# Performance work log

Measured on AMD Instinct MI355X. Metric: run time of the kernel, lower is better.

Reference implementation:

```python
import jax, jax.numpy as jnp
import numpy as np

N, E, D_IN, LAT = 50000, 600000, 128, 64


def setup_inputs() -> dict:
    key = jax.random.key(0)
    ks = jax.random.split(key, 16)

    def w(k, i, o):
        return jax.random.normal(k, (i, o), jnp.float32) * (1.0 / np.sqrt(i))

    dims = [(D_IN, 64), (64, 128), (128, LAT)]
    inp = {
        "x": jax.random.normal(ks[0], (N, D_IN), jnp.float32),
        "edge_index": jax.random.randint(ks[1], (2, E), 0, N),
        "eps": jax.random.normal(ks[2], (N, LAT), jnp.float32),
    }
    for b_i, branch in enumerate(["mu", "ls"]):
        for li, (i, o) in enumerate(dims):
            inp[f"w_{branch}{li+1}"] = w(ks[3 + b_i * 3 + li], i, o)
            inp[f"b_{branch}{li+1}"] = jnp.zeros((o,), jnp.float32)
    return inp


def gcn(x, src, dst, dis, W, b):
    # GCNConv with add_self_loops=True and symmetric normalization:
    # out = D^-1/2 (A + I) D^-1/2 (x W) + b
    h = x @ W
    norm = dis[src] * dis[dst]                       # [E]
    agg = jax.ops.segment_sum(h[src] * norm[:, None], dst, num_segments=N)
    agg = agg + h * (dis * dis)[:, None]             # self-loop term d_i^-1 * h_i
    return agg + b


def encode_branch(x, src, dst, dis, ws, bs):
    h = x
    for W, b in zip(ws, bs):
        h = jax.nn.relu(gcn(h, src, dst, dis, W, b))  # ReLU after every GCNConv
    return h


def reference(x, edge_index, eps,
              w_mu1, b_mu1, w_mu2, b_mu2, w_mu3, b_mu3,
              w_ls1, b_ls1, w_ls2, b_ls2, w_ls3, b_ls3):
    src, dst = edge_index[0], edge_index[1]
    # degree with self loops (edge_weight = 1)
    deg = jax.ops.segment_sum(jnp.ones(E, x.dtype), dst, num_segments=N) + 1.0
    dis = jax.lax.rsqrt(deg)
    mu = encode_branch(x, src, dst, dis, [w_mu1, w_mu2, w_mu3], [b_mu1, b_mu2, b_mu3])
    logstd = encode_branch(x, src, dst, dis, [w_ls1, w_ls2, w_ls3], [b_ls1, b_ls2, b_ls3])
    logstd = jnp.minimum(logstd, 10.0)               # PyG VGAE MAX_LOGSTD clamp
    z = mu + eps * jnp.exp(logstd)                   # reparametrize (training=True)
    # VGAE inner-product decoder on observed edges, sigmoid=True
    adj = jax.nn.sigmoid(jnp.sum(z[src] * z[dst], axis=-1))
    return adj, mu, logstd
```

## Files before the change

### kernel.cpp

```cpp
#include <hip/hip_runtime.h>
#include <hip/hip_bf16.h>
#include <hip/hip_fp16.h>
#include <math.h>


__global__ void zero_int_k(int* __restrict__ p, int n) {
    int i = blockIdx.x * blockDim.x + threadIdx.x;
    if (i < n) p[i] = 0;
}

__global__ void count_dst_k(const int* __restrict__ ei, int* __restrict__ cnt, int E) {
    int e = blockIdx.x * blockDim.x + threadIdx.x;
    if (e < E) atomicAdd(&cnt[ei[E + e]], 1);
}

__global__ void compute_dis_k(const int* __restrict__ cnt, float* __restrict__ dis, int n) {
    int i = blockIdx.x * blockDim.x + threadIdx.x;
    if (i < n) dis[i] = rsqrtf((float)cnt[i] + 1.0f);
}

__global__ void scan1_k(const int* __restrict__ cnt, int* __restrict__ row_ptr,
                        int* __restrict__ bsum, int n) {
    __shared__ int wsum[16];
    int tid = threadIdx.x, lane = tid & 63, wv = tid >> 6;
    int i = blockIdx.x * 1024 + tid;
    int v = (i < n) ? cnt[i] : 0;
    int x = v;
#pragma unroll
    for (int off = 1; off < 64; off <<= 1) {
        int t = __shfl_up(x, off, 64);
        if (lane >= off) x += t;
    }
    if (lane == 63) wsum[wv] = x;
    __syncthreads();
    if (wv == 0 && lane < 16) {
        int y = wsum[lane];
#pragma unroll
        for (int off = 1; off < 16; off <<= 1) {
            int t = __shfl_up(y, off, 64);
            if (lane >= off) y += t;
        }
        wsum[lane] = y;
    }
    __syncthreads();
    int incl = x + ((wv == 0) ? 0 : wsum[wv - 1]);
    if (i < n) row_ptr[i + 1] = incl;
    if (tid == 1023) bsum[blockIdx.x] = incl;
}

__global__ void scan2_k(int* __restrict__ bsum, int nb) {
    int lane = threadIdx.x;
    int v = (lane < nb) ? bsum[lane] : 0;
    int x = v;
#pragma unroll
    for (int off = 1; off < 64; off <<= 1) {
        int t = __shfl_up(x, off, 64);
        if (lane >= off) x += t;
    }
    if (lane < nb) bsum[lane] = x - v;
}

__global__ void scan3_k(const int* __restrict__ cnt, int* __restrict__ row_ptr,
                        const int* __restrict__ bsum, int* __restrict__ woff, int n) {
    int i = blockIdx.x * 1024 + threadIdx.x;
    if (i == 0) row_ptr[0] = 0;
    if (i < n) {
        int r = row_ptr[i + 1] + bsum[blockIdx.x];
        row_ptr[i + 1] = r;
        woff[i] = r - cnt[i];
    }
}

__global__ void scatter_edges_k(const int* __restrict__ ei, const float* __restrict__ dis,
                                int* __restrict__ woff, int* __restrict__ src_sorted,
                                float* __restrict__ norm_sorted, int E) {
    int e = blockIdx.x * blockDim.x + threadIdx.x;
    if (e < E) {
        int s = ei[e];
        int d = ei[E + e];
        int pos = atomicAdd(&woff[d], 1);
        src_sorted[pos]  = s;
        norm_sorted[pos] = dis[s] * dis[d];
    }
}

template <int K, int OUT, int EPI, int H16>
__global__ __launch_bounds__(256, 4) void matmul2_k(
        const float* __restrict__ AA, const float* __restrict__ AB, int lda,
        int offaA, int offaB,
        const float* __restrict__ WA, const float* __restrict__ WB,
        const float* __restrict__ bA, const float* __restrict__ bB,
        float* __restrict__ HA, float* __restrict__ HB, __half* __restrict__ HH,
        int ldh, int offhA, int offhB, int n) {
    constexpr int TX = OUT / 4;
    constexpr int TY = 256 / TX;
    constexpr int TM = TY * 4;
    constexpr int KC = 32, KC4 = 8;
    __shared__ float w_lds[K * OUT];
    __shared__ float a_lds[TM * KC];

    int by = blockIdx.y;
    const float* A  = by ? AB : AA;
    const float* W  = by ? WB : WA;
    const float* bi = by ? bB : bA;
    float*       H  = by ? HB : HA;
    int offa = by ? offaB : offaA;
    int offh = by ? offhB : offhA;

    int tid = threadIdx.x;
    for (int idx = tid; idx < K * OUT / 4; idx += 256)
        ((float4*)w_lds)[idx] = ((const float4*)W)[idx];

    int row0 = blockIdx.x * TM;
    int tx = tid % TX;
    int ty = tid / TX;

    float4 acc[4];
#pragma unroll
    for (int i = 0; i < 4; ++i) acc[i] = make_float4(0.f, 0.f, 0.f, 0.f);

    int abase[4], akey[4];
#pragma unroll
    for (int i = 0; i < 4; ++i) {
        int r = ty * 4 + i;
        abase[i] = r * KC;
        akey[i]  = (r >> 2) & 7;
    }

    for (int kc = 0; kc < K; kc += KC) {
        __syncthreads();
        for (int f4 = tid; f4 < TM * KC4; f4 += 256) {
            int row  = f4 >> 3;
            int col4 = f4 & 7;
            float4 v = make_float4(0.f, 0.f, 0.f, 0.f);
            if (row0 + row < n)
                v = *(const float4*)&A[(size_t)(row0 + row) * lda + offa + kc + (col4 << 2)];
            *(float4*)&a_lds[row * KC + ((col4 ^ ((row >> 2) & 7)) << 2)] = v;
        }
        __syncthreads();

#pragma unroll
        for (int k = 0; k < KC; k += 4) {
            int k4 = k >> 2;
            float af[4][4];
#pragma unroll
            for (int i = 0; i < 4; ++i) {
                float4 a = *(const float4*)&a_lds[abase[i] + ((k4 ^ akey[i]) << 2)];
                af[i][0] = a.x; af[i][1] = a.y; af[i][2] = a.z; af[i][3] = a.w;
            }
#pragma unroll
            for (int j = 0; j < 4; ++j) {
                float4 wv = ((const float4*)w_lds)[(kc + k + j) * TX + tx];
#pragma unroll
                for (int i = 0; i < 4; ++i) {
                    acc[i].x += af[i][j] * wv.x;
                    acc[i].y += af[i][j] * wv.y;
                    acc[i].z += af[i][j] * wv.z;
                    acc[i].w += af[i][j] * wv.w;
                }
            }
        }
    }

#pragma unroll
    for (int i = 0; i < 4; ++i) {
        int r = row0 + ty * 4 + i;
        if (r < n) {
            float4 o = acc[i];
            if (EPI == 1) {
                float4 b = ((const float4*)bi)[tx];
                o.x = fmaxf(o.x + b.x, 0.f);
                o.y = fmaxf(o.y + b.y, 0.f);
                o.z = fmaxf(o.z + b.z, 0.f);
                o.w = fmaxf(o.w + b.w, 0.f);
            }
            if (H16) {
                __half2 h0 = __floats2half2_rn(o.x, o.y);
                __half2 h1 = __floats2half2_rn(o.z, o.w);
                uint2 u = make_uint2(*(unsigned*)&h0, *(unsigned*)&h1);
                *(uint2*)&HH[(size_t)r * ldh + offh + tx * 4] = u;
            } else {
                *(float4*)&H[(size_t)r * ldh + offh + tx * 4] = o;
            }
        }
    }
}

template <int MODE>
__global__ void agg2h_k(const __half* __restrict__ h, const float* __restrict__ dis,
                        const int* __restrict__ row_ptr, const int* __restrict__ srcs,
                        const float* __restrict__ norms,
                        const float* __restrict__ bM, const float* __restrict__ bL,
                        const float* __restrict__ eps,
                        __half* __restrict__ oH, float* __restrict__ oI,
                        float* __restrict__ oM, float* __restrict__ oL,
                        float* __restrict__ z, int n) {
    int wid  = (int)((blockIdx.x * (size_t)blockDim.x + threadIdx.x) >> 6);
    int lane = threadIdx.x & 63;
    if (wid >= n) return;
    int g = lane >> 4;
    int q = lane & 15;
    const __half* hq = h + 8 * q;

    float acc[8];
#pragma unroll
    for (int i = 0; i < 8; ++i) acc[i] = 0.f;

    if (g == 0) {
        float di = dis[wid];
        float self = di * di;
        uint4 r = *(const uint4*)&hq[(size_t)wid * 128];
        const __half2* hp = (const __half2*)&r;
#pragma unroll
        for (int i = 0; i < 4; ++i) {
            float2 f = __half22float2(hp[i]);
            acc[2 * i]     = f.x * self;
            acc[2 * i + 1] = f.y * self;
        }
    }

    int beg = row_ptr[wid], end = row_ptr[wid + 1];
    for (int cb = beg; cb < end; cb += 64) {
        int m = end - cb;
        if (m > 64) m = 64;
        int sv = 0; float nv = 0.f;
        if (lane < m) { sv = srcs[cb + lane]; nv = norms[cb + lane]; }
        int j = 0;
        for (; j + 8 <= m; j += 8) {
            int   sA = __shfl(sv, j + g, 64);
            float wA = __shfl(nv, j + g, 64);
            int   sB = __shfl(sv, j + 4 + g, 64);
            float wB = __shfl(nv, j + 4 + g, 64);
            uint4 ra = *(const uint4*)&hq[(size_t)sA * 128];
            uint4 rb = *(const uint4*)&hq[(size_t)sB * 128];
            const __half2* pa = (const __half2*)&ra;
            const __half2* pb = (const __half2*)&rb;
#pragma unroll
            for (int i = 0; i < 4; ++i) {
                float2 fa = __half22float2(pa[i]);
                float2 fb = __half22float2(pb[i]);
                acc[2 * i]     = fmaf(fa.x, wA, acc[2 * i]);
                acc[2 * i + 1] = fmaf(fa.y, wA, acc[2 * i + 1]);
                acc[2 * i]     = fmaf(fb.x, wB, acc[2 * i]);
                acc[2 * i + 1] = fmaf(fb.y, wB, acc[2 * i + 1]);
            }
        }
        for (; j < m; j += 4) {
            int idx = j + g;
            int   sA = __shfl(sv, (idx < m) ? idx : j, 64);
            float wA = __shfl(nv, (idx < m) ? idx : j, 64);
            if (idx < m) {
                uint4 ra = *(const uint4*)&hq[(size_t)sA * 128];
                const __half2* pa = (const __half2*)&ra;
#pragma unroll
                for (int i = 0; i < 4; ++i) {
                    float2 fa = __half22float2(pa[i]);
                    acc[2 * i]     = fmaf(fa.x, wA, acc[2 * i]);
                    acc[2 * i + 1] = fmaf(fa.y, wA, acc[2 * i + 1]);
                }
            }
        }
    }

#pragma unroll
    for (int i = 0; i < 8; ++i) {
        acc[i] += __shfl_xor(acc[i], 16, 64);
        acc[i] += __shfl_xor(acc[i], 32, 64);
    }

    if (MODE == 0) {
        if (g == 0) {
            size_t rb = (size_t)wid * 128 + 8 * q;
            *(float4*)&oI[rb]     = make_float4(acc[0], acc[1], acc[2], acc[3]);
            *(float4*)&oI[rb + 4] = make_float4(acc[4], acc[5], acc[6], acc[7]);
        }
    } else if (MODE == 1) {
        if (g == 0) {
            const float* bs = (q < 8) ? bM + 8 * q : bL + 8 * q - 64;
            __half2 hh[4];
#pragma unroll
            for (int i = 0; i < 8; i += 2) {
                float a0 = fmaxf(acc[i] + bs[i], 0.f);
                float a1 = fmaxf(acc[i + 1] + bs[i + 1], 0.f);
                hh[i >> 1] = __floats2half2_rn(a0, a1);
            }
            *(uint4*)&oH[(size_t)wid * 128 + 8 * q] = *(uint4*)hh;
        }
    } else {
        const float* bs = (q < 8) ? bM + 8 * q : bL + 8 * q - 64;
        float act[8];
#pragma unroll
        for (int i = 0; i < 8; ++i) {
            float a = fmaxf(acc[i] + bs[i], 0.f);
            if (q >= 8) a = fminf(a, 10.f);
            act[i] = a;
        }
        float lsv[8];
#pragma unroll
        for (int i = 0; i < 8; ++i) lsv[i] = __shfl(act[i], lane + 8, 64);
        if (g == 0) {
            size_t ob = (size_t)wid * 64;
            if (q < 8) {
                *(float4*)&oM[ob + 8 * q]     = make_float4(act[0], act[1], act[2], act[3]);
                *(float4*)&oM[ob + 8 * q + 4] = make_float4(act[4], act[5], act[6], act[7]);
                float4 e0 = *(const float4*)&eps[ob + 8 * q];
                float4 e1 = *(const float4*)&eps[ob + 8 * q + 4];
                float4 z0, z1;
                z0.x = fmaf(e0.x, expf(lsv[0]), act[0]);
                z0.y = fmaf(e0.y, expf(lsv[1]), act[1]);
                z0.z = fmaf(e0.z, expf(lsv[2]), act[2]);
                z0.w = fmaf(e0.w, expf(lsv[3]), act[3]);
                z1.x = fmaf(e1.x, expf(lsv[4]), act[4]);
                z1.y = fmaf(e1.y, expf(lsv[5]), act[5]);
                z1.z = fmaf(e1.z, expf(lsv[6]), act[6]);
                z1.w = fmaf(e1.w, expf(lsv[7]), act[7]);
                *(float4*)&z[ob + 8 * q]     = z0;
                *(float4*)&z[ob + 8 * q + 4] = z1;
            } else {
                int qq = q - 8;
                *(float4*)&oL[ob + 8 * qq]     = make_float4(act[0], act[1], act[2], act[3]);
                *(float4*)&oL[ob + 8 * qq + 4] = make_float4(act[4], act[5], act[6], act[7]);
            }
        }
    }
}

__global__ void decoder_k(const int* __restrict__ ei, const float* __restrict__ z,
                          float* __restrict__ adj, int E) {
    int t = blockIdx.x * 256 + threadIdx.x;
    int e = t >> 4;
    int q = threadIdx.x & 15;
    if (e >= E) return;
    int s = ei[e];
    int d = ei[E + e];
    const float4* z4 = (const float4*)z;
    float4 a = z4[(size_t)s * 16 + q];
    float4 b = z4[(size_t)d * 16 + q];
    float p = a.x * b.x + a.y * b.y + a.z * b.z + a.w * b.w;
    p += __shfl_xor(p, 8);
    p += __shfl_xor(p, 4);
    p += __shfl_xor(p, 2);
    p += __shfl_xor(p, 1);
    if (q == 0) adj[e] = 1.f / (1.f + expf(-p));
}

extern "C" void kernel_launch(void* const* d_in, const int* in_sizes, int n_in,
                              void* d_out, int out_size, void* d_ws, size_t ws_size,
                              hipStream_t stream) {
    const float* x   = (const float*)d_in[0];
    const int*   ei  = (const int*)d_in[1];
    const float* eps = (const float*)d_in[2];
    const float* w_mu1 = (const float*)d_in[3];
    const float* b_mu1 = (const float*)d_in[4];
    const float* w_mu2 = (const float*)d_in[5];
    const float* b_mu2 = (const float*)d_in[6];
    const float* w_mu3 = (const float*)d_in[7];
    const float* b_mu3 = (const float*)d_in[8];
    const float* w_ls1 = (const float*)d_in[9];
    const float* b_ls1 = (const float*)d_in[10];
    const float* w_ls2 = (const float*)d_in[11];
    const float* b_ls2 = (const float*)d_in[12];
    const float* w_ls3 = (const float*)d_in[13];
    const float* b_ls3 = (const float*)d_in[14];

    const int N = in_sizes[0] / 128;
    const int E = in_sizes[1] / 2;
    const size_t NB = (size_t)N * 128;

    float* out = (float*)d_out;
    float* adj = out;
    float* mu  = out + E;
    float* ls  = out + E + (size_t)N * 64;
    float* M   = out + E;

    float* ws = (float*)d_ws;
    float*  R1  = ws;
    __half* hpA = (__half*)ws;
    float*  R3  = ws + NB;
    __half* hpB = (__half*)(ws + NB);
    float*  zb  = ws + NB;
    float* c0 = ws + 2 * NB;
    const size_t P  = 50176;
    const size_t EP = 600064;
    float* dis         = c0;
    int*   cnt         = (int*)(c0 + P);
    int*   row_ptr     = (int*)(c0 + 2 * P);
    int*   woff        = (int*)(c0 + 3 * P);
    int*   bsum        = (int*)(c0 + 4 * P);
    int*   src_sorted  = (int*)(c0 + 4 * P + 256);
    float* norm_sorted = c0 + 4 * P + 256 + EP;

    const int nscan = (N + 1023) / 1024;

    zero_int_k<<<(N + 255) / 256, 256, 0, stream>>>(cnt, N);
    count_dst_k<<<(E + 255) / 256, 256, 0, stream>>>(ei, cnt, E);
    compute_dis_k<<<(N + 255) / 256, 256, 0, stream>>>(cnt, dis, N);
    scan1_k<<<nscan, 1024, 0, stream>>>(cnt, row_ptr, bsum, N);
    scan2_k<<<1, 64, 0, stream>>>(bsum, nscan);
    scan3_k<<<nscan, 1024, 0, stream>>>(cnt, row_ptr, bsum, woff, N);
    scatter_edges_k<<<(E + 255) / 256, 256, 0, stream>>>(ei, dis, woff, src_sorted,
                                                         norm_sorted, E);

    const int aggBlocks = (int)(((size_t)N * 64 + 255) / 256);
    dim3 g64((N + 63) / 64, 2), g32((N + 31) / 32, 2);

    matmul2_k<128, 64, 0, 1><<<g64, 256, 0, stream>>>(x, x, 128, 0, 0, w_mu1, w_ls1,
                                                      nullptr, nullptr, nullptr, nullptr,
                                                      hpA, 128, 0, 64, N);
    agg2h_k<1><<<aggBlocks, 256, 0, stream>>>(hpA, dis, row_ptr, src_sorted, norm_sorted,
                                              b_mu1, b_ls1, nullptr, hpB, nullptr,
                                              nullptr, nullptr, nullptr, N);

    agg2h_k<0><<<aggBlocks, 256, 0, stream>>>(hpB, dis, row_ptr, src_sorted, norm_sorted,
                                              nullptr, nullptr, nullptr, nullptr, R1,
                                              nullptr, nullptr, nullptr, N);
    matmul2_k<64, 128, 1, 0><<<g32, 256, 0, stream>>>(R1, R1, 128, 0, 64, w_mu2, w_ls2,
                                                      b_mu2, b_ls2, M, R3, nullptr,
                                                      128, 0, 0, N);

    matmul2_k<128, 64, 0, 1><<<g64, 256, 0, stream>>>(M, R3, 128, 0, 0, w_mu3, w_ls3,
                                                      nullptr, nullptr, nullptr, nullptr,
                                                      hpA, 128, 0, 64, N);
    agg2h_k<2><<<aggBlocks, 256, 0, stream>>>(hpA, dis, row_ptr, src_sorted, norm_sorted,
                                              b_mu3, b_ls3, eps, nullptr, nullptr,
                                              mu, ls, zb, N);

    decoder_k<<<(int)(((size_t)E * 16 + 255) / 256), 256, 0, stream>>>(ei, zb, adj, E);
}
```

Before: 299.9 us.

## Factor symmetric GCN normalization into row scaling and store z in fp16

```diff
diff --git a/kernel.cpp b/kernel.cpp
--- a/kernel.cpp
+++ b/kernel.cpp
@@ -71,16 +71,14 @@
     }
 }
 
-__global__ void scatter_edges_k(const int* __restrict__ ei, const float* __restrict__ dis,
-                                int* __restrict__ woff, int* __restrict__ src_sorted,
-                                float* __restrict__ norm_sorted, int E) {
+__global__ void scatter_edges_k(const int* __restrict__ ei, int* __restrict__ woff,
+                                int* __restrict__ src_sorted, int E) {
     int e = blockIdx.x * blockDim.x + threadIdx.x;
     if (e < E) {
         int s = ei[e];
         int d = ei[E + e];
         int pos = atomicAdd(&woff[d], 1);
-        src_sorted[pos]  = s;
-        norm_sorted[pos] = dis[s] * dis[d];
+        src_sorted[pos] = s;
     }
 }
 
@@ -91,6 +89,7 @@
         const float* __restrict__ WA, const float* __restrict__ WB,
         const float* __restrict__ bA, const float* __restrict__ bB,
         float* __restrict__ HA, float* __restrict__ HB, __half* __restrict__ HH,
+        const float* __restrict__ dis,
         int ldh, int offhA, int offhB, int n) {
     constexpr int TX = OUT / 4;
     constexpr int TY = 256 / TX;
@@ -175,8 +174,9 @@
                 o.w = fmaxf(o.w + b.w, 0.f);
             }
             if (H16) {
-                __half2 h0 = __floats2half2_rn(o.x, o.y);
-                __half2 h1 = __floats2half2_rn(o.z, o.w);
+                float dsc = dis[r];
+                __half2 h0 = __floats2half2_rn(o.x * dsc, o.y * dsc);
+                __half2 h1 = __floats2half2_rn(o.z * dsc, o.w * dsc);
                 uint2 u = make_uint2(*(unsigned*)&h0, *(unsigned*)&h1);
                 *(uint2*)&HH[(size_t)r * ldh + offh + tx * 4] = u;
             } else {
@@ -189,12 +189,11 @@
 template <int MODE>
 __global__ void agg2h_k(const __half* __restrict__ h, const float* __restrict__ dis,
                         const int* __restrict__ row_ptr, const int* __restrict__ srcs,
-                        const float* __restrict__ norms,
                         const float* __restrict__ bM, const float* __restrict__ bL,
                         const float* __restrict__ eps,
                         __half* __restrict__ oH, float* __restrict__ oI,
                         float* __restrict__ oM, float* __restrict__ oL,
-                        float* __restrict__ z, int n) {
+                        __half* __restrict__ zh, int n) {
     int wid  = (int)((blockIdx.x * (size_t)blockDim.x + threadIdx.x) >> 6);
     int lane = threadIdx.x & 63;
     if (wid >= n) return;
@@ -207,15 +206,13 @@
     for (int i = 0; i < 8; ++i) acc[i] = 0.f;
 
     if (g == 0) {
-        float di = dis[wid];
-        float self = di * di;
         uint4 r = *(const uint4*)&hq[(size_t)wid * 128];
         const __half2* hp = (const __half2*)&r;
 #pragma unroll
         for (int i = 0; i < 4; ++i) {
             float2 f = __half22float2(hp[i]);
-            acc[2 * i]     = f.x * self;
-            acc[2 * i + 1] = f.y * self;
+            acc[2 * i]     = f.x;
+            acc[2 * i + 1] = f.y;
         }
     }
 
@@ -223,14 +220,12 @@
     for (int cb = beg; cb < end; cb += 64) {
         int m = end - cb;
         if (m > 64) m = 64;
-        int sv = 0; float nv = 0.f;
-        if (lane < m) { sv = srcs[cb + lane]; nv = norms[cb + lane]; }
+        int sv = 0;
+        if (lane < m) sv = srcs[cb + lane];
         int j = 0;
         for (; j + 8 <= m; j += 8) {
-            int   sA = __shfl(sv, j + g, 64);
-            float wA = __shfl(nv, j + g, 64);
-            int   sB = __shfl(sv, j + 4 + g, 64);
-            float wB = __shfl(nv, j + 4 + g, 64);
+            int sA = __shfl(sv, j + g, 64);
+            int sB = __shfl(sv, j + 4 + g, 64);
             uint4 ra = *(const uint4*)&hq[(size_t)sA * 128];
             uint4 rb = *(const uint4*)&hq[(size_t)sB * 128];
             const __half2* pa = (const __half2*)&ra;
@@ -239,24 +234,21 @@
             for (int i = 0; i < 4; ++i) {
                 float2 fa = __half22float2(pa[i]);
                 float2 fb = __half22float2(pb[i]);
-                acc[2 * i]     = fmaf(fa.x, wA, acc[2 * i]);
-                acc[2 * i + 1] = fmaf(fa.y, wA, acc[2 * i + 1]);
-                acc[2 * i]     = fmaf(fb.x, wB, acc[2 * i]);
-                acc[2 * i + 1] = fmaf(fb.y, wB, acc[2 * i + 1]);
+                acc[2 * i]     += fa.x + fb.x;
+                acc[2 * i + 1] += fa.y + fb.y;
             }
         }
         for (; j < m; j += 4) {
             int idx = j + g;
-            int   sA = __shfl(sv, (idx < m) ? idx : j, 64);
-            float wA = __shfl(nv, (idx < m) ? idx : j, 64);
+            int sA = __shfl(sv, (idx < m) ? idx : j, 64);
             if (idx < m) {
                 uint4 ra = *(const uint4*)&hq[(size_t)sA * 128];
                 const __half2* pa = (const __half2*)&ra;
 #pragma unroll
                 for (int i = 0; i < 4; ++i) {
                     float2 fa = __half22float2(pa[i]);
-                    acc[2 * i]     = fmaf(fa.x, wA, acc[2 * i]);
-                    acc[2 * i + 1] = fmaf(fa.y, wA, acc[2 * i + 1]);
+                    acc[2 * i]     += fa.x;
+                    acc[2 * i + 1] += fa.y;
                 }
             }
         }
@@ -267,6 +259,10 @@
         acc[i] += __shfl_xor(acc[i], 16, 64);
         acc[i] += __shfl_xor(acc[i], 32, 64);
     }
+
+    float di = dis[wid];
+#pragma unroll
+    for (int i = 0; i < 8; ++i) acc[i] *= di;
 
     if (MODE == 0) {
         if (g == 0) {
@@ -280,8 +276,8 @@
             __half2 hh[4];
 #pragma unroll
             for (int i = 0; i < 8; i += 2) {
-                float a0 = fmaxf(acc[i] + bs[i], 0.f);
-                float a1 = fmaxf(acc[i + 1] + bs[i + 1], 0.f);
+                float a0 = fmaxf(acc[i] + bs[i], 0.f) * di;
+                float a1 = fmaxf(acc[i + 1] + bs[i + 1], 0.f) * di;
                 hh[i >> 1] = __floats2half2_rn(a0, a1);
             }
             *(uint4*)&oH[(size_t)wid * 128 + 8 * q] = *(uint4*)hh;
@@ -305,17 +301,19 @@
                 *(float4*)&oM[ob + 8 * q + 4] = make_float4(act[4], act[5], act[6], act[7]);
                 float4 e0 = *(const float4*)&eps[ob + 8 * q];
                 float4 e1 = *(const float4*)&eps[ob + 8 * q + 4];
-                float4 z0, z1;
-                z0.x = fmaf(e0.x, expf(lsv[0]), act[0]);
-                z0.y = fmaf(e0.y, expf(lsv[1]), act[1]);
-                z0.z = fmaf(e0.z, expf(lsv[2]), act[2]);
-                z0.w = fmaf(e0.w, expf(lsv[3]), act[3]);
-                z1.x = fmaf(e1.x, expf(lsv[4]), act[4]);
-                z1.y = fmaf(e1.y, expf(lsv[5]), act[5]);
-                z1.z = fmaf(e1.z, expf(lsv[6]), act[6]);
-                z1.w = fmaf(e1.w, expf(lsv[7]), act[7]);
-                *(float4*)&z[ob + 8 * q]     = z0;
-                *(float4*)&z[ob + 8 * q + 4] = z1;
+                float zz[8];
+                zz[0] = fmaf(e0.x, expf(lsv[0]), act[0]);
+                zz[1] = fmaf(e0.y, expf(lsv[1]), act[1]);
+                zz[2] = fmaf(e0.z, expf(lsv[2]), act[2]);
+                zz[3] = fmaf(e0.w, expf(lsv[3]), act[3]);
+                zz[4] = fmaf(e1.x, expf(lsv[4]), act[4]);
+                zz[5] = fmaf(e1.y, expf(lsv[5]), act[5]);
+                zz[6] = fmaf(e1.z, expf(lsv[6]), act[6]);
+                zz[7] = fmaf(e1.w, expf(lsv[7]), act[7]);
+                __half2 zh4[4];
+#pragma unroll
+                for (int i = 0; i < 4; ++i) zh4[i] = __floats2half2_rn(zz[2 * i], zz[2 * i + 1]);
+                *(uint4*)&zh[ob + 8 * q] = *(uint4*)zh4;
             } else {
                 int qq = q - 8;
                 *(float4*)&oL[ob + 8 * qq]     = make_float4(act[0], act[1], act[2], act[3]);
@@ -325,7 +323,7 @@
     }
 }
 
-__global__ void decoder_k(const int* __restrict__ ei, const float* __restrict__ z,
+__global__ void decoder_k(const int* __restrict__ ei, const __half* __restrict__ zh,
                           float* __restrict__ adj, int E) {
     int t = blockIdx.x * 256 + threadIdx.x;
     int e = t >> 4;
@@ -333,10 +331,19 @@
     if (e >= E) return;
     int s = ei[e];
     int d = ei[E + e];
-    const float4* z4 = (const float4*)z;
-    float4 a = z4[(size_t)s * 16 + q];
-    float4 b = z4[(size_t)d * 16 + q];
-    float p = a.x * b.x + a.y * b.y + a.z * b.z + a.w * b.w;
+    const uint2* z2 = (const uint2*)zh;
+    uint2 ua = z2[(size_t)s * 16 + q];
+    uint2 ub = z2[(size_t)d * 16 + q];
+    const __half2* pa = (const __half2*)&ua;
+    const __half2* pb = (const __half2*)&ub;
+    float p = 0.f;
+#pragma unroll
+    for (int i = 0; i < 2; ++i) {
+        float2 fa = __half22float2(pa[i]);
+        float2 fb = __half22float2(pb[i]);
+        p = fmaf(fa.x, fb.x, p);
+        p = fmaf(fa.y, fb.y, p);
+    }
     p += __shfl_xor(p, 8);
     p += __shfl_xor(p, 4);
     p += __shfl_xor(p, 2);
@@ -378,17 +385,15 @@
     __half* hpA = (__half*)ws;
     float*  R3  = ws + NB;
     __half* hpB = (__half*)(ws + NB);
-    float*  zb  = ws + NB;
+    __half* zh  = (__half*)(ws + NB);
     float* c0 = ws + 2 * NB;
-    const size_t P  = 50176;
-    const size_t EP = 600064;
+    const size_t P = 50176;
     float* dis         = c0;
     int*   cnt         = (int*)(c0 + P);
     int*   row_ptr     = (int*)(c0 + 2 * P);
     int*   woff        = (int*)(c0 + 3 * P);
     int*   bsum        = (int*)(c0 + 4 * P);
     int*   src_sorted  = (int*)(c0 + 4 * P + 256);
-    float* norm_sorted = c0 + 4 * P + 256 + EP;
 
     const int nscan = (N + 1023) / 1024;
 
@@ -398,32 +403,31 @@
     scan1_k<<<nscan, 1024, 0, stream>>>(cnt, row_ptr, bsum, N);
     scan2_k<<<1, 64, 0, stream>>>(bsum, nscan);
     scan3_k<<<nscan, 1024, 0, stream>>>(cnt, row_ptr, bsum, woff, N);
-    scatter_edges_k<<<(E + 255) / 256, 256, 0, stream>>>(ei, dis, woff, src_sorted,
-                                                         norm_sorted, E);
+    scatter_edges_k<<<(E + 255) / 256, 256, 0, stream>>>(ei, woff, src_sorted, E);
 
     const int aggBlocks = (int)(((size_t)N * 64 + 255) / 256);
     dim3 g64((N + 63) / 64, 2), g32((N + 31) / 32, 2);
 
     matmul2_k<128, 64, 0, 1><<<g64, 256, 0, stream>>>(x, x, 128, 0, 0, w_mu1, w_ls1,
                                                       nullptr, nullptr, nullptr, nullptr,
-                                                      hpA, 128, 0, 64, N);
-    agg2h_k<1><<<aggBlocks, 256, 0, stream>>>(hpA, dis, row_ptr, src_sorted, norm_sorted,
+                                                      hpA, dis, 128, 0, 64, N);
+    agg2h_k<1><<<aggBlocks, 256, 0, stream>>>(hpA, dis, row_ptr, src_sorted,
                                               b_mu1, b_ls1, nullptr, hpB, nullptr,
                                               nullptr, nullptr, nullptr, N);
 
-    agg2h_k<0><<<aggBlocks, 256, 0, stream>>>(hpB, dis, row_ptr, src_sorted, norm_sorted,
+    agg2h_k<0><<<aggBlocks, 256, 0, stream>>>(hpB, dis, row_ptr, src_sorted,
                                               nullptr, nullptr, nullptr, nullptr, R1,
                                               nullptr, nullptr, nullptr, N);
     matmul2_k<64, 128, 1, 0><<<g32, 256, 0, stream>>>(R1, R1, 128, 0, 64, w_mu2, w_ls2,
-                                                      b_mu2, b_ls2, M, R3, nullptr,
+                                                      b_mu2, b_ls2, M, R3, nullptr, nullptr,
                                                       128, 0, 0, N);
 
     matmul2_k<128, 64, 0, 1><<<g64, 256, 0, stream>>>(M, R3, 128, 0, 0, w_mu3, w_ls3,
                                                       nullptr, nullptr, nullptr, nullptr,
-                                                      hpA, 128, 0, 64, N);
-    agg2h_k<2><<<aggBlocks, 256, 0, stream>>>(hpA, dis, row_ptr, src_sorted, norm_sorted,
+                                                      hpA, dis, 128, 0, 64, N);
+    agg2h_k<2><<<aggBlocks, 256, 0, stream>>>(hpA, dis, row_ptr, src_sorted,
                                               b_mu3, b_ls3, eps, nullptr, nullptr,
-                                              mu, ls, zb, N);
-
-    decoder_k<<<(int)(((size_t)E * 16 + 255) / 256), 256, 0, stream>>>(ei, zb, adj, E);
-}
+                                              mu, ls, zh, N);
+
+    decoder_k<<<(int)(((size_t)E * 16 + 255) / 256), 256, 0, stream>>>(ei, zh, adj, E);
+}
```

After: 283.8 us. 5.4% less time.
